# Kernel optimization log

Hardware: AMD Instinct MI355X
Metric: run time of the kernel (lower is better)

## Reference

```python
import jax, jax.numpy as jnp
import numpy as np

B, H, S, D = 2, 16, 2048, 64

def setup_inputs() -> dict:
    key = jax.random.key(0)
    kq, kk, kv = jax.random.split(key, 3)
    query = jax.random.normal(kq, (B, H, S, D), dtype=jnp.float32)
    k_ = jax.random.normal(kk, (B, H, S, D), dtype=jnp.float32)
    value = jax.random.normal(kv, (B, H, S, D), dtype=jnp.float32)
    # causal 0/1 mask, broadcasts over batch/head dims
    mask = jnp.tril(jnp.ones((S, S), dtype=jnp.float32))
    return {"query": query, "key": k_, "value": value, "mask": mask}

def reference(query, key, value, mask):
    scale = 1.0 / jnp.sqrt(jnp.asarray(query.shape[-1], query.dtype))
    # [B,H,Sq,Sk] score matrix (naive, fully materialized like the original)
    scores = jnp.einsum('bhqd,bhkd->bhqk', query, key) * scale
    scores = jnp.where(mask == 0, -jnp.inf, scores)
    attn = jax.nn.softmax(scores, axis=-1)
    return jnp.einsum('bhqk,bhkd->bhqd', attn, value)
```

## Files before the change

kernel.cpp:

```cpp
#include <hip/hip_runtime.h>
#include <hip/hip_bf16.h>
#include <math.h>

typedef __attribute__((ext_vector_type(4)))  float f32x4;
typedef __attribute__((ext_vector_type(16))) float f32x16;
typedef __attribute__((ext_vector_type(8)))  short bf16x8;
typedef __attribute__((ext_vector_type(4)))  short bf16x4;

#define S_SZ 2048
#define D_SZ 64

constexpr int KVBLK = 64;
constexpr int KP  = 72;
constexpr int NQT = 16;
constexpr int OFP = 68;
constexpr float SCL2 = 0.18033688011112042f;
constexpr float DEFER_THR = 44.0f;

struct Smem {
    short Kt[2][KVBLK][KP];
    short Vt[2][4096];
};
union SmemU {
    Smem s;
    float Of[256][OFP];
};

__device__ __forceinline__ short f2bf(float f) {
    union { __hip_bfloat16 h; short s; } u;
    u.h = __float2bfloat16(f);
    return u.s;
}
__device__ __forceinline__ unsigned cvt_pk_bf16(float lo, float hi) {
    unsigned r;
    asm("v_cvt_pk_bf16_f32 %0, %1, %2" : "=v"(r) : "v"(lo), "v"(hi));
    return r;
}
#define PSWAP(a, b) asm("v_permlane32_swap_b32 %0, %1" : "+v"(a), "+v"(b))
#define TRREAD(dst, addr, off) \
    asm volatile("ds_read_b64_tr_b16 %0, %1 offset:" #off : "=v"(dst) : "v"(addr))

__device__ __forceinline__ bf16x8 cat(bf16x4 a, bf16x4 b) {
    return __builtin_shufflevector(a, b, 0, 1, 2, 3, 4, 5, 6, 7);
}

__global__ __launch_bounds__(512, 2)
void attn_fwd(const float* __restrict__ Q, const float* __restrict__ K,
              const float* __restrict__ V, float* __restrict__ O)
{
    __shared__ __align__(16) SmemU u;
    Smem* sm = &u.s;

    const int tid  = threadIdx.x;
    const int wid  = tid >> 6;
    const int lane = tid & 63;
    const int lq   = lane & 31;
    const int h    = lane >> 5;

    const int b    = blockIdx.x;
    const int xcd  = b & 7;
    const int i    = b >> 3;
    const int p    = i & 7;
    const int head = xcd + 8 * (i >> 3);

    const int grp   = wid >> 2;
    const int wq    = wid & 3;
    const int qt_my = grp ? (NQT - 1 - p) : p;
    const int qbase = qt_my * 128 + wq * 32;
    const int qglob = qbase + lq;
    const int nT    = 2 * (NQT - 1 - p) + 2;

    const size_t hoff = (size_t)head * S_SZ * D_SZ;
    const float* Qh = Q + hoff;
    const float* Kh = K + hoff;
    const float* Vh = V + hoff;
    float*       Oh = O + hoff;

    const int skv = tid >> 3;
    const int sd0 = (tid & 7) * 8;
    const int vC  = (tid & 7) >> 1;
    const int vR  = skv >> 2;
    const int vt_off = (vC * 16 + vR) * 64 + (skv & 3) * 16 + (tid & 1) * 8;

    const int cg = (lane >> 4) & 1;
    const unsigned vtbase = (unsigned)(uintptr_t)&sm->Vt[0][0]
                          + (unsigned)cg * 2048u + (unsigned)h * 256u
                          + (unsigned)(lane & 15) * 8u;

    bf16x8 qfrag[4];
    {
        const float* qrow = Qh + (size_t)qglob * D_SZ;
        #pragma unroll
        for (int dc = 0; dc < 4; ++dc) {
            const float* ptr = qrow + dc * 16 + h * 8;
            f32x4 a = *(const f32x4*)ptr;
            f32x4 c = *(const f32x4*)(ptr + 4);
            bf16x8 q;
            q[0]=f2bf(a[0]); q[1]=f2bf(a[1]); q[2]=f2bf(a[2]); q[3]=f2bf(a[3]);
            q[4]=f2bf(c[0]); q[5]=f2bf(c[1]); q[6]=f2bf(c[2]); q[7]=f2bf(c[3]);
            qfrag[dc] = q;
        }
    }

    f32x16 oa0, oa1;
    #pragma unroll
    for (int r = 0; r < 16; ++r) { oa0[r] = 0.f; oa1[r] = 0.f; }
    float m_run = -INFINITY, l_run = 0.f;

    f32x4 kreg[2], vreg[2];

    {
        const float* ksrc = Kh + (size_t)skv * D_SZ + sd0;
        const float* vsrc = Vh + (size_t)skv * D_SZ + sd0;
        kreg[0] = ((const f32x4*)ksrc)[0]; kreg[1] = ((const f32x4*)ksrc)[1];
        vreg[0] = ((const f32x4*)vsrc)[0]; vreg[1] = ((const f32x4*)vsrc)[1];
    }
    {
        bf16x8 pk;
        pk[0]=f2bf(kreg[0][0]); pk[1]=f2bf(kreg[0][1]); pk[2]=f2bf(kreg[0][2]); pk[3]=f2bf(kreg[0][3]);
        pk[4]=f2bf(kreg[1][0]); pk[5]=f2bf(kreg[1][1]); pk[6]=f2bf(kreg[1][2]); pk[7]=f2bf(kreg[1][3]);
        *(bf16x8*)&sm->Kt[0][skv][sd0] = pk;
        bf16x8 pv;
        pv[0]=f2bf(vreg[0][0]); pv[1]=f2bf(vreg[0][1]); pv[2]=f2bf(vreg[0][2]); pv[3]=f2bf(vreg[0][3]);
        pv[4]=f2bf(vreg[1][0]); pv[5]=f2bf(vreg[1][1]); pv[6]=f2bf(vreg[1][2]); pv[7]=f2bf(vreg[1][3]);
        *(bf16x8*)&sm->Vt[0][vt_off] = pv;
    }
    __syncthreads();

    for (int t = 0; t < nT; ++t) {
        const int buf = t & 1;

        if (t + 1 < nT) {
            const int kb = (t + 1) * KVBLK;
            const float* ksrc = Kh + (size_t)(kb + skv) * D_SZ + sd0;
            const float* vsrc = Vh + (size_t)(kb + skv) * D_SZ + sd0;
            kreg[0] = ((const f32x4*)ksrc)[0]; kreg[1] = ((const f32x4*)ksrc)[1];
            vreg[0] = ((const f32x4*)vsrc)[0]; vreg[1] = ((const f32x4*)vsrc)[1];
        }

        if (64 * t < qbase + 32) {
            f32x16 st0, st1;
            #pragma unroll
            for (int r = 0; r < 16; ++r) { st0[r] = 0.f; st1[r] = 0.f; }
            __builtin_amdgcn_s_setprio(1);
            #pragma unroll
            for (int dc = 0; dc < 4; ++dc) {
                bf16x8 kf0 = *(const bf16x8*)&sm->Kt[buf][lq     ][dc * 16 + h * 8];
                bf16x8 kf1 = *(const bf16x8*)&sm->Kt[buf][32 + lq][dc * 16 + h * 8];
                st0 = __builtin_amdgcn_mfma_f32_32x32x16_bf16(kf0, qfrag[dc], st0, 0, 0, 0);
                st1 = __builtin_amdgcn_mfma_f32_32x32x16_bf16(kf1, qfrag[dc], st1, 0, 0, 0);
            }
            __builtin_amdgcn_s_setprio(0);

            const unsigned va = vtbase + (buf ? 8192u : 0u);
            bf16x4 t00,t01,t10,t11,t20,t21,t30,t31;
            bf16x4 u00,u01,u10,u11,u20,u21,u30,u31;
            TRREAD(t00, va, 0);    TRREAD(t01, va, 128);
            TRREAD(t10, va, 512);  TRREAD(t11, va, 640);
            TRREAD(t20, va, 1024); TRREAD(t21, va, 1152);
            TRREAD(t30, va, 1536); TRREAD(t31, va, 1664);
            TRREAD(u00, va, 4096); TRREAD(u01, va, 4224);
            TRREAD(u10, va, 4608); TRREAD(u11, va, 4736);
            TRREAD(u20, va, 5120); TRREAD(u21, va, 5248);
            TRREAD(u30, va, 5632); TRREAD(u31, va, 5760);

            if (64 * t + 63 > qbase) {
                #pragma unroll
                for (int r = 0; r < 16; ++r) {
                    const int k0 = 64 * t + (r & 3) + 8 * (r >> 2) + 4 * h;
                    if (k0      > qglob) st0[r] = -INFINITY;
                    if (k0 + 32 > qglob) st1[r] = -INFINITY;
                }
            }

            float pmax = -INFINITY;
            #pragma unroll
            for (int r = 0; r < 16; ++r) {
                pmax = fmaxf(pmax, st0[r]);
                pmax = fmaxf(pmax, st1[r]);
            }
            pmax = fmaxf(pmax, __shfl_xor(pmax, 32));

            if (!__all(pmax - m_run <= DEFER_THR)) {
                const float mnew  = fmaxf(m_run, pmax);
                const float alpha = __builtin_amdgcn_exp2f((m_run - mnew) * SCL2);
                m_run = mnew;
                l_run *= alpha;
                #pragma unroll
                for (int r = 0; r < 16; ++r) { oa0[r] *= alpha; oa1[r] *= alpha; }
            }
            const float mb = m_run * SCL2;

            float psum = 0.f;
            #pragma unroll
            for (int r = 0; r < 16; ++r) {
                st0[r] = __builtin_amdgcn_exp2f(fmaf(st0[r], SCL2, -mb));
                st1[r] = __builtin_amdgcn_exp2f(fmaf(st1[r], SCL2, -mb));
                psum += st0[r] + st1[r];
            }
            psum += __shfl_xor(psum, 32);
            l_run += psum;

            bf16x8 pfrag[4];
            {
                unsigned w0, w1, w2, w3;
                w0 = cvt_pk_bf16(st0[0], st0[1]);  w1 = cvt_pk_bf16(st0[2], st0[3]);
                w2 = cvt_pk_bf16(st0[4], st0[5]);  w3 = cvt_pk_bf16(st0[6], st0[7]);
                PSWAP(w0, w2); PSWAP(w1, w3);
                { union { unsigned uu[4]; bf16x8 v; } ww = {{w0, w1, w2, w3}}; pfrag[0] = ww.v; }
                w0 = cvt_pk_bf16(st0[8], st0[9]);  w1 = cvt_pk_bf16(st0[10], st0[11]);
                w2 = cvt_pk_bf16(st0[12], st0[13]);w3 = cvt_pk_bf16(st0[14], st0[15]);
                PSWAP(w0, w2); PSWAP(w1, w3);
                { union { unsigned uu[4]; bf16x8 v; } ww = {{w0, w1, w2, w3}}; pfrag[1] = ww.v; }
                w0 = cvt_pk_bf16(st1[0], st1[1]);  w1 = cvt_pk_bf16(st1[2], st1[3]);
                w2 = cvt_pk_bf16(st1[4], st1[5]);  w3 = cvt_pk_bf16(st1[6], st1[7]);
                PSWAP(w0, w2); PSWAP(w1, w3);
                { union { unsigned uu[4]; bf16x8 v; } ww = {{w0, w1, w2, w3}}; pfrag[2] = ww.v; }
                w0 = cvt_pk_bf16(st1[8], st1[9]);  w1 = cvt_pk_bf16(st1[10], st1[11]);
                w2 = cvt_pk_bf16(st1[12], st1[13]);w3 = cvt_pk_bf16(st1[14], st1[15]);
                PSWAP(w0, w2); PSWAP(w1, w3);
                { union { unsigned uu[4]; bf16x8 v; } ww = {{w0, w1, w2, w3}}; pfrag[3] = ww.v; }
            }

            asm volatile("s_waitcnt lgkmcnt(0)" ::: "memory");
            __builtin_amdgcn_sched_barrier(0);

            __builtin_amdgcn_s_setprio(1);
            oa0 = __builtin_amdgcn_mfma_f32_32x32x16_bf16(cat(t00, t01), pfrag[0], oa0, 0, 0, 0);
            oa0 = __builtin_amdgcn_mfma_f32_32x32x16_bf16(cat(t10, t11), pfrag[1], oa0, 0, 0, 0);
            oa0 = __builtin_amdgcn_mfma_f32_32x32x16_bf16(cat(t20, t21), pfrag[2], oa0, 0, 0, 0);
            oa0 = __builtin_amdgcn_mfma_f32_32x32x16_bf16(cat(t30, t31), pfrag[3], oa0, 0, 0, 0);
            oa1 = __builtin_amdgcn_mfma_f32_32x32x16_bf16(cat(u00, u01), pfrag[0], oa1, 0, 0, 0);
            oa1 = __builtin_amdgcn_mfma_f32_32x32x16_bf16(cat(u10, u11), pfrag[1], oa1, 0, 0, 0);
            oa1 = __builtin_amdgcn_mfma_f32_32x32x16_bf16(cat(u20, u21), pfrag[2], oa1, 0, 0, 0);
            oa1 = __builtin_amdgcn_mfma_f32_32x32x16_bf16(cat(u30, u31), pfrag[3], oa1, 0, 0, 0);
            __builtin_amdgcn_s_setprio(0);
        }

        if (t + 1 < nT) {
            const int nb = buf ^ 1;
            bf16x8 pk;
            pk[0]=f2bf(kreg[0][0]); pk[1]=f2bf(kreg[0][1]); pk[2]=f2bf(kreg[0][2]); pk[3]=f2bf(kreg[0][3]);
            pk[4]=f2bf(kreg[1][0]); pk[5]=f2bf(kreg[1][1]); pk[6]=f2bf(kreg[1][2]); pk[7]=f2bf(kreg[1][3]);
            *(bf16x8*)&sm->Kt[nb][skv][sd0] = pk;
            bf16x8 pv;
            pv[0]=f2bf(vreg[0][0]); pv[1]=f2bf(vreg[0][1]); pv[2]=f2bf(vreg[0][2]); pv[3]=f2bf(vreg[0][3]);
            pv[4]=f2bf(vreg[1][0]); pv[5]=f2bf(vreg[1][1]); pv[6]=f2bf(vreg[1][2]); pv[7]=f2bf(vreg[1][3]);
            *(bf16x8*)&sm->Vt[nb][vt_off] = pv;
        }
        __syncthreads();
    }

    const float inv = 1.f / l_run;
    {
        const int orow = grp * 128 + wq * 32 + lq;
        #pragma unroll
        for (int s = 0; s < 4; ++s) {
            f32x4 w0, w1;
            #pragma unroll
            for (int j = 0; j < 4; ++j) { w0[j] = oa0[4*s+j] * inv; w1[j] = oa1[4*s+j] * inv; }
            *(f32x4*)&u.Of[orow][     s * 8 + 4 * h] = w0;
            *(f32x4*)&u.Of[orow][32 + s * 8 + 4 * h] = w1;
        }
    }
    __syncthreads();
    {
        const int g2 = tid >> 8;
        const int r2 = (tid & 255) >> 1;
        const int c2 = (tid & 1) * 32;
        const int qt2 = g2 ? (NQT - 1 - p) : p;
        float* dst = Oh + (size_t)(qt2 * 128 + r2) * D_SZ + c2;
        const float* src = &u.Of[g2 * 128 + r2][c2];
        #pragma unroll
        for (int j = 0; j < 8; ++j)
            ((f32x4*)dst)[j] = ((const f32x4*)src)[j];
    }
}

extern "C" void kernel_launch(void* const* d_in, const int* in_sizes, int n_in,
                              void* d_out, int out_size, void* d_ws, size_t ws_size,
                              hipStream_t stream) {
    const float* Q = (const float*)d_in[0];
    const float* K = (const float*)d_in[1];
    const float* V = (const float*)d_in[2];
    float* Ou = (float*)d_out;
    attn_fwd<<<dim3(256), 512, 0, stream>>>(Q, K, V, Ou);
}
```

Before: 52.45 us.

## Split KV range across two wave groups per query tile and merge partial softmax

Each block now handles a single 128-row query tile instead of a pair of complementary tiles. Its two wave groups each take half of a 128-wide KV block and process it in parallel. The partial max/sum/output from the two groups are merged through shared memory at the end. The grid doubles to 512 blocks with heavier tiles issued first, and launch bounds now ask for 4 blocks per CU. The aim is more parallelism and better load balance across CUs, at the cost of an extra cross-group reduction, more register pressure, and no longer pairing tiles for causal balance.

```diff
diff --git a/kernel.cpp b/kernel.cpp
--- a/kernel.cpp
+++ b/kernel.cpp
@@ -10,20 +10,23 @@
 #define S_SZ 2048
 #define D_SZ 64
 
-constexpr int KVBLK = 64;
+constexpr int KVBLK = 128;
 constexpr int KP  = 72;
 constexpr int NQT = 16;
-constexpr int OFP = 68;
 constexpr float SCL2 = 0.18033688011112042f;
 constexpr float DEFER_THR = 44.0f;
 
 struct Smem {
     short Kt[2][KVBLK][KP];
-    short Vt[2][4096];
+    short Vt[2][8192];
 };
 union SmemU {
     Smem s;
-    float Of[256][OFP];
+    struct {
+        float Om[128][66];
+        float Mm[2][128];
+        float Lm[2][128];
+    } e;
 };
 
 __device__ __forceinline__ short f2bf(float f) {
@@ -44,7 +47,7 @@
     return __builtin_shufflevector(a, b, 0, 1, 2, 3, 4, 5, 6, 7);
 }
 
-__global__ __launch_bounds__(512, 2)
+__global__ __launch_bounds__(512, 4)
 void attn_fwd(const float* __restrict__ Q, const float* __restrict__ K,
               const float* __restrict__ V, float* __restrict__ O)
 {
@@ -58,17 +61,19 @@
     const int h    = lane >> 5;
 
     const int b    = blockIdx.x;
-    const int xcd  = b & 7;
-    const int i    = b >> 3;
-    const int p    = i & 7;
-    const int head = xcd + 8 * (i >> 3);
-
-    const int grp   = wid >> 2;
-    const int wq    = wid & 3;
-    const int qt_my = grp ? (NQT - 1 - p) : p;
-    const int qbase = qt_my * 128 + wq * 32;
+    const int pass = b >> 8;
+    const int c    = b & 255;
+    const int xcd  = c & 7;
+    const int i2   = c >> 3;
+    const int j    = i2 & 7;
+    const int head = xcd + 8 * (i2 >> 3);
+    const int qt   = pass ? j : (NQT - 1 - j);
+
+    const int grp  = wid >> 2;
+    const int wq   = wid & 3;
+    const int qbase = qt * 128 + wq * 32;
     const int qglob = qbase + lq;
-    const int nT    = 2 * (NQT - 1 - p) + 2;
+    const int nT    = qt + 1;
 
     const size_t hoff = (size_t)head * S_SZ * D_SZ;
     const float* Qh = Q + hoff;
@@ -76,16 +81,14 @@
     const float* Vh = V + hoff;
     float*       Oh = O + hoff;
 
-    const int skv = tid >> 3;
-    const int sd0 = (tid & 7) * 8;
-    const int vC  = (tid & 7) >> 1;
-    const int vR  = skv >> 2;
-    const int vt_off = (vC * 16 + vR) * 64 + (skv & 3) * 16 + (tid & 1) * 8;
+    const int kr   = tid >> 2;
+    const int kc0  = (tid & 3) * 16;
+    const int vt_off = ((tid & 3) * 32 + (kr >> 2)) * 64 + (kr & 3) * 16;
 
     const int cg = (lane >> 4) & 1;
     const unsigned vtbase = (unsigned)(uintptr_t)&sm->Vt[0][0]
-                          + (unsigned)cg * 2048u + (unsigned)h * 256u
-                          + (unsigned)(lane & 15) * 8u;
+                          + (unsigned)grp * 2048u + (unsigned)cg * 4096u
+                          + (unsigned)h * 256u + (unsigned)(lane & 15) * 8u;
 
     bf16x8 qfrag[4];
     {
@@ -93,11 +96,11 @@
         #pragma unroll
         for (int dc = 0; dc < 4; ++dc) {
             const float* ptr = qrow + dc * 16 + h * 8;
-            f32x4 a = *(const f32x4*)ptr;
-            f32x4 c = *(const f32x4*)(ptr + 4);
+            f32x4 a0 = *(const f32x4*)ptr;
+            f32x4 a1 = *(const f32x4*)(ptr + 4);
             bf16x8 q;
-            q[0]=f2bf(a[0]); q[1]=f2bf(a[1]); q[2]=f2bf(a[2]); q[3]=f2bf(a[3]);
-            q[4]=f2bf(c[0]); q[5]=f2bf(c[1]); q[6]=f2bf(c[2]); q[7]=f2bf(c[3]);
+            q[0]=f2bf(a0[0]); q[1]=f2bf(a0[1]); q[2]=f2bf(a0[2]); q[3]=f2bf(a0[3]);
+            q[4]=f2bf(a1[0]); q[5]=f2bf(a1[1]); q[6]=f2bf(a1[2]); q[7]=f2bf(a1[3]);
             qfrag[dc] = q;
         }
     }
@@ -107,67 +110,67 @@
     for (int r = 0; r < 16; ++r) { oa0[r] = 0.f; oa1[r] = 0.f; }
     float m_run = -INFINITY, l_run = 0.f;
 
-    f32x4 kreg[2], vreg[2];
+    f32x4 kreg[4], vreg[4];
 
     {
-        const float* ksrc = Kh + (size_t)skv * D_SZ + sd0;
-        const float* vsrc = Vh + (size_t)skv * D_SZ + sd0;
-        kreg[0] = ((const f32x4*)ksrc)[0]; kreg[1] = ((const f32x4*)ksrc)[1];
-        vreg[0] = ((const f32x4*)vsrc)[0]; vreg[1] = ((const f32x4*)vsrc)[1];
-    }
-    {
-        bf16x8 pk;
-        pk[0]=f2bf(kreg[0][0]); pk[1]=f2bf(kreg[0][1]); pk[2]=f2bf(kreg[0][2]); pk[3]=f2bf(kreg[0][3]);
-        pk[4]=f2bf(kreg[1][0]); pk[5]=f2bf(kreg[1][1]); pk[6]=f2bf(kreg[1][2]); pk[7]=f2bf(kreg[1][3]);
-        *(bf16x8*)&sm->Kt[0][skv][sd0] = pk;
-        bf16x8 pv;
-        pv[0]=f2bf(vreg[0][0]); pv[1]=f2bf(vreg[0][1]); pv[2]=f2bf(vreg[0][2]); pv[3]=f2bf(vreg[0][3]);
-        pv[4]=f2bf(vreg[1][0]); pv[5]=f2bf(vreg[1][1]); pv[6]=f2bf(vreg[1][2]); pv[7]=f2bf(vreg[1][3]);
-        *(bf16x8*)&sm->Vt[0][vt_off] = pv;
+        const float* ksrc = Kh + (size_t)kr * D_SZ + kc0;
+        const float* vsrc = Vh + (size_t)kr * D_SZ + kc0;
+        #pragma unroll
+        for (int q2 = 0; q2 < 4; ++q2) { kreg[q2] = ((const f32x4*)ksrc)[q2]; vreg[q2] = ((const f32x4*)vsrc)[q2]; }
+        bf16x8 p0, p1;
+        p0[0]=f2bf(kreg[0][0]); p0[1]=f2bf(kreg[0][1]); p0[2]=f2bf(kreg[0][2]); p0[3]=f2bf(kreg[0][3]);
+        p0[4]=f2bf(kreg[1][0]); p0[5]=f2bf(kreg[1][1]); p0[6]=f2bf(kreg[1][2]); p0[7]=f2bf(kreg[1][3]);
+        p1[0]=f2bf(kreg[2][0]); p1[1]=f2bf(kreg[2][1]); p1[2]=f2bf(kreg[2][2]); p1[3]=f2bf(kreg[2][3]);
+        p1[4]=f2bf(kreg[3][0]); p1[5]=f2bf(kreg[3][1]); p1[6]=f2bf(kreg[3][2]); p1[7]=f2bf(kreg[3][3]);
+        *(bf16x8*)&sm->Kt[0][kr][kc0]     = p0;
+        *(bf16x8*)&sm->Kt[0][kr][kc0 + 8] = p1;
+        bf16x8 v0, v1;
+        v0[0]=f2bf(vreg[0][0]); v0[1]=f2bf(vreg[0][1]); v0[2]=f2bf(vreg[0][2]); v0[3]=f2bf(vreg[0][3]);
+        v0[4]=f2bf(vreg[1][0]); v0[5]=f2bf(vreg[1][1]); v0[6]=f2bf(vreg[1][2]); v0[7]=f2bf(vreg[1][3]);
+        v1[0]=f2bf(vreg[2][0]); v1[1]=f2bf(vreg[2][1]); v1[2]=f2bf(vreg[2][2]); v1[3]=f2bf(vreg[2][3]);
+        v1[4]=f2bf(vreg[3][0]); v1[5]=f2bf(vreg[3][1]); v1[6]=f2bf(vreg[3][2]); v1[7]=f2bf(vreg[3][3]);
+        *(bf16x8*)&sm->Vt[0][vt_off]     = v0;
+        *(bf16x8*)&sm->Vt[0][vt_off + 8] = v1;
     }
     __syncthreads();
 
     for (int t = 0; t < nT; ++t) {
         const int buf = t & 1;
+        const int kmin = 128 * t + grp * 64;
+        const bool active = kmin <= qbase + 31;
 
         if (t + 1 < nT) {
-            const int kb = (t + 1) * KVBLK;
-            const float* ksrc = Kh + (size_t)(kb + skv) * D_SZ + sd0;
-            const float* vsrc = Vh + (size_t)(kb + skv) * D_SZ + sd0;
-            kreg[0] = ((const f32x4*)ksrc)[0]; kreg[1] = ((const f32x4*)ksrc)[1];
-            vreg[0] = ((const f32x4*)vsrc)[0]; vreg[1] = ((const f32x4*)vsrc)[1];
-        }
-
-        if (64 * t < qbase + 32) {
-            f32x16 st0, st1;
+            const float* ksrc = Kh + (size_t)((t + 1) * KVBLK + kr) * D_SZ + kc0;
+            #pragma unroll
+            for (int q2 = 0; q2 < 4; ++q2) kreg[q2] = ((const f32x4*)ksrc)[q2];
+        }
+
+        f32x16 st0, st1;
+        if (active) {
             #pragma unroll
             for (int r = 0; r < 16; ++r) { st0[r] = 0.f; st1[r] = 0.f; }
             __builtin_amdgcn_s_setprio(1);
             #pragma unroll
             for (int dc = 0; dc < 4; ++dc) {
-                bf16x8 kf0 = *(const bf16x8*)&sm->Kt[buf][lq     ][dc * 16 + h * 8];
-                bf16x8 kf1 = *(const bf16x8*)&sm->Kt[buf][32 + lq][dc * 16 + h * 8];
+                bf16x8 kf0 = *(const bf16x8*)&sm->Kt[buf][grp * 64 + lq     ][dc * 16 + h * 8];
+                bf16x8 kf1 = *(const bf16x8*)&sm->Kt[buf][grp * 64 + 32 + lq][dc * 16 + h * 8];
                 st0 = __builtin_amdgcn_mfma_f32_32x32x16_bf16(kf0, qfrag[dc], st0, 0, 0, 0);
                 st1 = __builtin_amdgcn_mfma_f32_32x32x16_bf16(kf1, qfrag[dc], st1, 0, 0, 0);
             }
             __builtin_amdgcn_s_setprio(0);
-
-            const unsigned va = vtbase + (buf ? 8192u : 0u);
-            bf16x4 t00,t01,t10,t11,t20,t21,t30,t31;
-            bf16x4 u00,u01,u10,u11,u20,u21,u30,u31;
-            TRREAD(t00, va, 0);    TRREAD(t01, va, 128);
-            TRREAD(t10, va, 512);  TRREAD(t11, va, 640);
-            TRREAD(t20, va, 1024); TRREAD(t21, va, 1152);
-            TRREAD(t30, va, 1536); TRREAD(t31, va, 1664);
-            TRREAD(u00, va, 4096); TRREAD(u01, va, 4224);
-            TRREAD(u10, va, 4608); TRREAD(u11, va, 4736);
-            TRREAD(u20, va, 5120); TRREAD(u21, va, 5248);
-            TRREAD(u30, va, 5632); TRREAD(u31, va, 5760);
-
-            if (64 * t + 63 > qbase) {
+        }
+
+        if (t + 1 < nT) {
+            const float* vsrc = Vh + (size_t)((t + 1) * KVBLK + kr) * D_SZ + kc0;
+            #pragma unroll
+            for (int q2 = 0; q2 < 4; ++q2) vreg[q2] = ((const f32x4*)vsrc)[q2];
+        }
+
+        if (active) {
+            if (kmin + 63 > qbase) {
                 #pragma unroll
                 for (int r = 0; r < 16; ++r) {
-                    const int k0 = 64 * t + (r & 3) + 8 * (r >> 2) + 4 * h;
+                    const int k0 = kmin + (r & 3) + 8 * (r >> 2) + 4 * h;
                     if (k0      > qglob) st0[r] = -INFINITY;
                     if (k0 + 32 > qglob) st1[r] = -INFINITY;
                 }
@@ -204,24 +207,35 @@
             bf16x8 pfrag[4];
             {
                 unsigned w0, w1, w2, w3;
-                w0 = cvt_pk_bf16(st0[0], st0[1]);  w1 = cvt_pk_bf16(st0[2], st0[3]);
-                w2 = cvt_pk_bf16(st0[4], st0[5]);  w3 = cvt_pk_bf16(st0[6], st0[7]);
+                w0 = cvt_pk_bf16(st0[0], st0[1]);   w1 = cvt_pk_bf16(st0[2], st0[3]);
+                w2 = cvt_pk_bf16(st0[4], st0[5]);   w3 = cvt_pk_bf16(st0[6], st0[7]);
                 PSWAP(w0, w2); PSWAP(w1, w3);
                 { union { unsigned uu[4]; bf16x8 v; } ww = {{w0, w1, w2, w3}}; pfrag[0] = ww.v; }
-                w0 = cvt_pk_bf16(st0[8], st0[9]);  w1 = cvt_pk_bf16(st0[10], st0[11]);
-                w2 = cvt_pk_bf16(st0[12], st0[13]);w3 = cvt_pk_bf16(st0[14], st0[15]);
+                w0 = cvt_pk_bf16(st0[8], st0[9]);   w1 = cvt_pk_bf16(st0[10], st0[11]);
+                w2 = cvt_pk_bf16(st0[12], st0[13]); w3 = cvt_pk_bf16(st0[14], st0[15]);
                 PSWAP(w0, w2); PSWAP(w1, w3);
                 { union { unsigned uu[4]; bf16x8 v; } ww = {{w0, w1, w2, w3}}; pfrag[1] = ww.v; }
-                w0 = cvt_pk_bf16(st1[0], st1[1]);  w1 = cvt_pk_bf16(st1[2], st1[3]);
-                w2 = cvt_pk_bf16(st1[4], st1[5]);  w3 = cvt_pk_bf16(st1[6], st1[7]);
+                w0 = cvt_pk_bf16(st1[0], st1[1]);   w1 = cvt_pk_bf16(st1[2], st1[3]);
+                w2 = cvt_pk_bf16(st1[4], st1[5]);   w3 = cvt_pk_bf16(st1[6], st1[7]);
                 PSWAP(w0, w2); PSWAP(w1, w3);
                 { union { unsigned uu[4]; bf16x8 v; } ww = {{w0, w1, w2, w3}}; pfrag[2] = ww.v; }
-                w0 = cvt_pk_bf16(st1[8], st1[9]);  w1 = cvt_pk_bf16(st1[10], st1[11]);
-                w2 = cvt_pk_bf16(st1[12], st1[13]);w3 = cvt_pk_bf16(st1[14], st1[15]);
+                w0 = cvt_pk_bf16(st1[8], st1[9]);   w1 = cvt_pk_bf16(st1[10], st1[11]);
+                w2 = cvt_pk_bf16(st1[12], st1[13]); w3 = cvt_pk_bf16(st1[14], st1[15]);
                 PSWAP(w0, w2); PSWAP(w1, w3);
                 { union { unsigned uu[4]; bf16x8 v; } ww = {{w0, w1, w2, w3}}; pfrag[3] = ww.v; }
             }
 
+            const unsigned va = vtbase + (buf ? 16384u : 0u);
+            bf16x4 t00,t01,t10,t11,t20,t21,t30,t31;
+            bf16x4 u00,u01,u10,u11,u20,u21,u30,u31;
+            TRREAD(t00, va, 0);    TRREAD(t01, va, 128);
+            TRREAD(t10, va, 512);  TRREAD(t11, va, 640);
+            TRREAD(t20, va, 1024); TRREAD(t21, va, 1152);
+            TRREAD(t30, va, 1536); TRREAD(t31, va, 1664);
+            TRREAD(u00, va, 8192); TRREAD(u01, va, 8320);
+            TRREAD(u10, va, 8704); TRREAD(u11, va, 8832);
+            TRREAD(u20, va, 9216); TRREAD(u21, va, 9344);
+            TRREAD(u30, va, 9728); TRREAD(u31, va, 9856);
             asm volatile("s_waitcnt lgkmcnt(0)" ::: "memory");
             __builtin_amdgcn_sched_barrier(0);
 
@@ -239,41 +253,69 @@
 
         if (t + 1 < nT) {
             const int nb = buf ^ 1;
-            bf16x8 pk;
-            pk[0]=f2bf(kreg[0][0]); pk[1]=f2bf(kreg[0][1]); pk[2]=f2bf(kreg[0][2]); pk[3]=f2bf(kreg[0][3]);
-            pk[4]=f2bf(kreg[1][0]); pk[5]=f2bf(kreg[1][1]); pk[6]=f2bf(kreg[1][2]); pk[7]=f2bf(kreg[1][3]);
-            *(bf16x8*)&sm->Kt[nb][skv][sd0] = pk;
-            bf16x8 pv;
-            pv[0]=f2bf(vreg[0][0]); pv[1]=f2bf(vreg[0][1]); pv[2]=f2bf(vreg[0][2]); pv[3]=f2bf(vreg[0][3]);
-            pv[4]=f2bf(vreg[1][0]); pv[5]=f2bf(vreg[1][1]); pv[6]=f2bf(vreg[1][2]); pv[7]=f2bf(vreg[1][3]);
-            *(bf16x8*)&sm->Vt[nb][vt_off] = pv;
+            bf16x8 p0, p1;
+            p0[0]=f2bf(kreg[0][0]); p0[1]=f2bf(kreg[0][1]); p0[2]=f2bf(kreg[0][2]); p0[3]=f2bf(kreg[0][3]);
+            p0[4]=f2bf(kreg[1][0]); p0[5]=f2bf(kreg[1][1]); p0[6]=f2bf(kreg[1][2]); p0[7]=f2bf(kreg[1][3]);
+            p1[0]=f2bf(kreg[2][0]); p1[1]=f2bf(kreg[2][1]); p1[2]=f2bf(kreg[2][2]); p1[3]=f2bf(kreg[2][3]);
+            p1[4]=f2bf(kreg[3][0]); p1[5]=f2bf(kreg[3][1]); p1[6]=f2bf(kreg[3][2]); p1[7]=f2bf(kreg[3][3]);
+            *(bf16x8*)&sm->Kt[nb][kr][kc0]     = p0;
+            *(bf16x8*)&sm->Kt[nb][kr][kc0 + 8] = p1;
+            bf16x8 v0, v1;
+            v0[0]=f2bf(vreg[0][0]); v0[1]=f2bf(vreg[0][1]); v0[2]=f2bf(vreg[0][2]); v0[3]=f2bf(vreg[0][3]);
+            v0[4]=f2bf(vreg[1][0]); v0[5]=f2bf(vreg[1][1]); v0[6]=f2bf(vreg[1][2]); v0[7]=f2bf(vreg[1][3]);
+            v1[0]=f2bf(vreg[2][0]); v1[1]=f2bf(vreg[2][1]); v1[2]=f2bf(vreg[2][2]); v1[3]=f2bf(vreg[2][3]);
+            v1[4]=f2bf(vreg[3][0]); v1[5]=f2bf(vreg[3][1]); v1[6]=f2bf(vreg[3][2]); v1[7]=f2bf(vreg[3][3]);
+            *(bf16x8*)&sm->Vt[nb][vt_off]     = v0;
+            *(bf16x8*)&sm->Vt[nb][vt_off + 8] = v1;
         }
         __syncthreads();
     }
 
-    const float inv = 1.f / l_run;
-    {
-        const int orow = grp * 128 + wq * 32 + lq;
-        #pragma unroll
-        for (int s = 0; s < 4; ++s) {
-            f32x4 w0, w1;
-            #pragma unroll
-            for (int j = 0; j < 4; ++j) { w0[j] = oa0[4*s+j] * inv; w1[j] = oa1[4*s+j] * inv; }
-            *(f32x4*)&u.Of[orow][     s * 8 + 4 * h] = w0;
-            *(f32x4*)&u.Of[orow][32 + s * 8 + 4 * h] = w1;
-        }
-    }
+    const int qv = wq * 32 + lq;
+    if (h == 0) { u.e.Mm[grp][qv] = m_run; u.e.Lm[grp][qv] = l_run; }
     __syncthreads();
     {
-        const int g2 = tid >> 8;
-        const int r2 = (tid & 255) >> 1;
-        const int c2 = (tid & 1) * 32;
-        const int qt2 = g2 ? (NQT - 1 - p) : p;
-        float* dst = Oh + (size_t)(qt2 * 128 + r2) * D_SZ + c2;
-        const float* src = &u.Of[g2 * 128 + r2][c2];
+        const float mA = u.e.Mm[0][qv], mB = u.e.Mm[1][qv];
+        const float lA = u.e.Lm[0][qv], lB = u.e.Lm[1][qv];
+        const float mX = fmaxf(mA, mB);
+        const float aA = __builtin_amdgcn_exp2f((mA - mX) * SCL2);
+        const float aB = __builtin_amdgcn_exp2f((mB - mX) * SCL2);
+        const float linv = 1.f / (lA * aA + lB * aB);
+        const float scl = (grp ? aB : aA) * linv;
+
+        if (grp == 0) {
+            #pragma unroll
+            for (int s = 0; s < 4; ++s) {
+                f32x4 w0, w1;
+                #pragma unroll
+                for (int j2 = 0; j2 < 4; ++j2) { w0[j2] = oa0[4*s+j2] * scl; w1[j2] = oa1[4*s+j2] * scl; }
+                *(f32x4*)&u.e.Om[qv][     s * 8 + 4 * h] = w0;
+                *(f32x4*)&u.e.Om[qv][32 + s * 8 + 4 * h] = w1;
+            }
+        }
+        __syncthreads();
+        if (grp == 1) {
+            #pragma unroll
+            for (int s = 0; s < 4; ++s) {
+                f32x4 w0 = *(const f32x4*)&u.e.Om[qv][     s * 8 + 4 * h];
+                f32x4 w1 = *(const f32x4*)&u.e.Om[qv][32 + s * 8 + 4 * h];
+                #pragma unroll
+                for (int j2 = 0; j2 < 4; ++j2) { w0[j2] += oa0[4*s+j2] * scl; w1[j2] += oa1[4*s+j2] * scl; }
+                *(f32x4*)&u.e.Om[qv][     s * 8 + 4 * h] = w0;
+                *(f32x4*)&u.e.Om[qv][32 + s * 8 + 4 * h] = w1;
+            }
+        }
+        __syncthreads();
+    }
+
+    {
+        const int row = tid >> 2;
+        const int c0  = (tid & 3) * 16;
+        float* dst = Oh + (size_t)(qt * 128 + row) * D_SZ + c0;
+        const float* src = &u.e.Om[row][c0];
         #pragma unroll
-        for (int j = 0; j < 8; ++j)
-            ((f32x4*)dst)[j] = ((const f32x4*)src)[j];
+        for (int j2 = 0; j2 < 4; ++j2)
+            ((f32x4*)dst)[j2] = ((const f32x4*)src)[j2];
     }
 }
 
@@ -284,5 +326,5 @@
     const float* K = (const float*)d_in[1];
     const float* V = (const float*)d_in[2];
     float* Ou = (float*)d_out;
-    attn_fwd<<<dim3(256), 512, 0, stream>>>(Q, K, V, Ou);
-}
+    attn_fwd<<<dim3(512), 512, 0, stream>>>(Q, K, V, Ou);
+}
```

Measured after the change: 128.5 us. 2.45x slower.
